# Performance work log

Measured on AMD Instinct MI355X. Metric: run time of the kernel, lower is better.

Reference implementation:

```python
import jax, jax.numpy as jnp
import numpy as np

N = 50000       # nodes
E = 1_200_000   # directed edges (avg degree 24)
IN_F = 128
C = 64          # CL1_F hidden width
K = 3           # Chebyshev order
OUT_F = 2
EPS = 1e-5      # BatchNorm eps (torch default)


def setup_inputs() -> dict:
    key = jax.random.key(0)
    ks = jax.random.split(key, 8)
    s = 0.1
    x = jax.random.normal(ks[0], (N, IN_F), dtype=jnp.float32)
    edge_index = jax.random.randint(ks[1], (2, E), 0, N, dtype=jnp.int32)
    W1 = jax.random.normal(ks[2], (K, IN_F, C), dtype=jnp.float32) * s
    b1 = jnp.zeros((C,), jnp.float32)
    W_rest = jax.random.normal(ks[3], (9, K, C, C), dtype=jnp.float32) * s
    b_rest = jnp.zeros((9, C), jnp.float32)
    gamma = jnp.ones((10, C), jnp.float32)
    beta = jnp.zeros((10, C), jnp.float32)
    lin_w = jax.random.normal(ks[4], (C, OUT_F), dtype=jnp.float32) * s
    lin_b = jnp.zeros((OUT_F,), jnp.float32)
    return dict(x=x, edge_index=edge_index, W1=W1, b1=b1, W_rest=W_rest,
                b_rest=b_rest, gamma=gamma, beta=beta, lin_w=lin_w, lin_b=lin_b)


def _cheb_norm(edge_index):
    # PyG ChebConv normalization with lambda_max=2, sym Laplacian, unit edge weights:
    # L_hat = 2L/lambda_max - I = -D^{-1/2} A D^{-1/2} (diagonal becomes 0).
    row, col = edge_index[0], edge_index[1]
    deg = jax.ops.segment_sum(jnp.ones((E,), jnp.float32), row, num_segments=N)
    dinv = jnp.where(deg > 0, jax.lax.rsqrt(jnp.maximum(deg, 1.0)), 0.0)
    w = -dinv[row] * dinv[col]  # per-edge weight of L_hat
    return row, col, w


def _cheb_conv(x, W, b, row, col, w):
    # Chebyshev recursion: Tx_0 = x, Tx_1 = L_hat x, Tx_k = 2 L_hat Tx_{k-1} - Tx_{k-2}
    Lhat = lambda v: jax.ops.segment_sum(w[:, None] * v[col], row, num_segments=N)
    Tx0 = x
    out = Tx0 @ W[0]
    Tx1 = Lhat(x)
    out = out + Tx1 @ W[1]
    for k in range(2, W.shape[0]):
        Tx2 = 2.0 * Lhat(Tx1) - Tx0
        out = out + Tx2 @ W[k]
        Tx0, Tx1 = Tx1, Tx2
    return out + b


def _bn(x, g, b):
    # BatchNorm1d over nodes (training-mode batch statistics, biased var)
    mu = x.mean(axis=0)
    var = ((x - mu) ** 2).mean(axis=0)
    return g * (x - mu) * jax.lax.rsqrt(var + EPS) + b


def reference(x, edge_index, W1, b1, W_rest, b_rest, gamma, beta, lin_w, lin_b):
    row, col, w = _cheb_norm(edge_index)
    h = _bn(jax.nn.relu(_cheb_conv(x, W1, b1, row, col, w)), gamma[0], beta[0])
    for i in range(9):  # convs 2..10 (structurally identical, stacked params)
        h = _bn(jax.nn.relu(_cheb_conv(h, W_rest[i], b_rest[i], row, col, w)),
                gamma[i + 1], beta[i + 1])
    return h @ lin_w + lin_b
```

## Files before the change

### kernel.cpp

```cpp
#include <hip/hip_runtime.h>
#include <hip/hip_bf16.h>

#define N_NODES 50000
#define N_EDGES 1200000
#define EPS_BN 1e-5f
#define NB 1024
#define RPB 49
#define CAP 2048

typedef __attribute__((ext_vector_type(8))) short short8;
typedef __attribute__((ext_vector_type(4))) float f32x4;

union U16x8 { uint4 u; short8 s; };

__device__ __forceinline__ float lo2f(unsigned int u){ return __uint_as_float(u << 16); }
__device__ __forceinline__ float hi2f(unsigned int u){ return __uint_as_float(u & 0xffff0000u); }
__device__ __forceinline__ float b2f(unsigned short u){ return __uint_as_float(((unsigned int)u) << 16); }
__device__ __forceinline__ unsigned short f2b(float f){
  __hip_bfloat16 b = __float2bfloat16(f);
  return __builtin_bit_cast(unsigned short, b);
}

__global__ void binA(const int* __restrict__ row, const int* __restrict__ col,
                     int* __restrict__ bcnt, int2* __restrict__ tmp, int E){
  __shared__ int hist[NB];
  __shared__ int base[NB];
  for (int i=threadIdx.x; i<NB; i+=256) hist[i] = 0;
  __syncthreads();
  int e0 = blockIdx.x*4096;
  int r_[16], c_[16];
  #pragma unroll
  for (int k=0;k<16;k++){
    int e = e0 + k*256 + threadIdx.x;
    if (e < E){
      r_[k] = row[e]; c_[k] = col[e];
      atomicAdd(&hist[r_[k]/RPB], 1);
    } else r_[k] = -1;
  }
  __syncthreads();
  for (int i=threadIdx.x; i<NB; i+=256){
    int cnt = hist[i];
    base[i] = cnt ? atomicAdd(&bcnt[i], cnt) : 0;
    hist[i] = 0;
  }
  __syncthreads();
  #pragma unroll
  for (int k=0;k<16;k++){
    if (r_[k] >= 0){
      int b = r_[k]/RPB;
      int p = base[b] + atomicAdd(&hist[b], 1);
      tmp[(size_t)b*CAP + p] = make_int2(r_[k], c_[k]);
    }
  }
}

__global__ void scan1024(const int* __restrict__ bcnt, int* __restrict__ bbase,
                         int* __restrict__ offs, int n, int E){
  __shared__ int tmp[NB];
  int i = threadIdx.x;
  int v = bcnt[i];
  tmp[i] = v;
  __syncthreads();
  for (int off=1; off<NB; off<<=1){
    int t = (i >= off) ? tmp[i-off] : 0;
    __syncthreads();
    tmp[i] += t;
    __syncthreads();
  }
  bbase[i] = tmp[i] - v;
  if (i == 0) offs[n] = E;
}

__global__ void binB(const int* __restrict__ bcnt, const int* __restrict__ bbase,
                     const int2* __restrict__ tmp,
                     int* __restrict__ offs, float* __restrict__ dinv,
                     int* __restrict__ ep, int n){
  __shared__ int cnt[RPB];
  __shared__ int roff[RPB];
  int b = blockIdx.x;
  int r0 = b*RPB;
  int m = bcnt[b];
  size_t tbase = (size_t)b*CAP;
  for (int i=threadIdx.x; i<RPB; i+=256) cnt[i] = 0;
  __syncthreads();
  for (int t=threadIdx.x; t<m; t+=256)
    atomicAdd(&cnt[tmp[tbase+t].x - r0], 1);
  __syncthreads();
  if (threadIdx.x == 0){
    int acc = bbase[b];
    #pragma unroll
    for (int i=0;i<RPB;i++){ roff[i] = acc; acc += cnt[i]; }
  }
  __syncthreads();
  if (threadIdx.x < RPB){
    int r = r0 + threadIdx.x;
    if (r < n){
      offs[r] = roff[threadIdx.x];
      int d = cnt[threadIdx.x];
      dinv[r] = (d>0) ? rsqrtf((float)d) : 0.f;
    }
  }
  __syncthreads();
  for (int i=threadIdx.x; i<RPB; i+=256) cnt[i] = 0;
  __syncthreads();
  for (int t=threadIdx.x; t<m; t+=256){
    int2 rc = tmp[tbase+t];
    int lr = rc.x - r0;
    int p = roff[lr] + atomicAdd(&cnt[lr], 1);
    ep[p] = rc.y;
  }
}

__global__ void cast_xs(const float* __restrict__ x, const float* __restrict__ dinv,
                        uint4* __restrict__ xs, int n){
  int t = blockIdx.x*256 + threadIdx.x;
  if (t >= n*16) return;
  int node = t >> 4;
  int fb = (t & 15)*8;
  float dv = dinv[node];
  const float* xp = x + (size_t)node*128 + fb;
  float4 v0 = *(const float4*)xp;
  float4 v1 = *(const float4*)(xp+4);
  float vv[8] = {v0.x,v0.y,v0.z,v0.w,v1.x,v1.y,v1.z,v1.w};
  uint4 o;
  unsigned int* op = (unsigned int*)&o;
  #pragma unroll
  for (int p=0;p<4;p++){
    op[p] = (unsigned int)f2b(dv*vv[2*p]) | ((unsigned int)f2b(dv*vv[2*p+1]) << 16);
  }
  xs[t] = o;
}

__global__ void transpose_w_split(const float* __restrict__ W1, const float* __restrict__ Wr,
                                  unsigned short* __restrict__ WTh,
                                  unsigned short* __restrict__ WTl){
  int t = blockIdx.x*256 + threadIdx.x;
  float val;
  if (t < 24576){
    int c = t/384, kk = t%384;
    int seg = kk/128, f = kk%128;
    if (seg==0)      val = W1[(size_t)f*64 + c] - W1[(size_t)(256+f)*64 + c];
    else if (seg==1) val = W1[(size_t)(128+f)*64 + c];
    else             val = 2.f * W1[(size_t)(256+f)*64 + c];
  } else if (t < 135168){
    int u = t - 24576;
    int L = u/12288, r2 = u%12288;
    int c = r2/192, kk = r2%192;
    int seg = kk/64, f = kk%64;
    const float* WL = Wr + (size_t)L*12288;
    if (seg==0)      val = WL[(size_t)f*64 + c] - WL[(size_t)(128+f)*64 + c];
    else if (seg==1) val = WL[(size_t)(64+f)*64 + c];
    else             val = 2.f * WL[(size_t)(128+f)*64 + c];
  } else return;
  unsigned short h = f2b(val);
  WTh[t] = h;
  WTl[t] = f2b(val - b2f(h));
}

__device__ __forceinline__ void spmm_acc8(uint4 u, float* a){
  a[0] += lo2f(u.x);
  a[1] += hi2f(u.x);
  a[2] += lo2f(u.y);
  a[3] += hi2f(u.y);
  a[4] += lo2f(u.z);
  a[5] += hi2f(u.z);
  a[6] += lo2f(u.w);
  a[7] += hi2f(u.w);
}

template<int F, bool BOTH>
__global__ void spmm_bf16(const int* __restrict__ offs, const int* __restrict__ ep,
                          const float* __restrict__ dinv,
                          const unsigned short* __restrict__ src,
                          unsigned short* __restrict__ dst_u,
                          unsigned short* __restrict__ dst_s, int n){
  constexpr int LPR = F/8;
  constexpr int RPW = 64/LPR;
  int lane = threadIdx.x & 63;
  int wv = threadIdx.x >> 6;
  int lr = lane / LPR;
  int li = lane % LPR;
  int row = (blockIdx.x*4 + wv)*RPW + lr;
  int s = 0, e = 0;
  if (row < n){ s = offs[row]; e = offs[row+1]; }
  float a[8];
  #pragma unroll
  for (int c=0;c<8;c++) a[c]=0.f;
  const int fb = li*8;
  int j = s;
  for (; j+4 <= e; j += 4){
    int c0 = ep[j+0];
    int c1 = ep[j+1];
    int c2 = ep[j+2];
    int c3 = ep[j+3];
    uint4 u0 = *(const uint4*)(src + (size_t)c0*F + fb);
    uint4 u1 = *(const uint4*)(src + (size_t)c1*F + fb);
    uint4 u2 = *(const uint4*)(src + (size_t)c2*F + fb);
    uint4 u3 = *(const uint4*)(src + (size_t)c3*F + fb);
    spmm_acc8(u0, a);
    spmm_acc8(u1, a);
    spmm_acc8(u2, a);
    spmm_acc8(u3, a);
  }
  for (; j < e; ++j){
    uint4 u = *(const uint4*)(src + (size_t)ep[j]*F + fb);
    spmm_acc8(u, a);
  }
  if (row < n){
    float dv = dinv[row];
    float uv[8];
    #pragma unroll
    for (int c=0;c<8;c++) uv[c] = -dv * a[c];
    uint4 ou;
    unsigned int* oup = (unsigned int*)&ou;
    #pragma unroll
    for (int p=0;p<4;p++)
      oup[p] = (unsigned int)f2b(uv[2*p]) | ((unsigned int)f2b(uv[2*p+1]) << 16);
    *(uint4*)(dst_u + (size_t)row*F + fb) = ou;
    if (BOTH){
      uint4 os;
      unsigned int* osp = (unsigned int*)&os;
      #pragma unroll
      for (int p=0;p<4;p++)
        osp[p] = (unsigned int)f2b(dv*uv[2*p]) | ((unsigned int)f2b(dv*uv[2*p+1]) << 16);
      *(uint4*)(dst_s + (size_t)row*F + fb) = os;
    }
  }
}

template<int SEGF>
__global__ void gemm_mfma(const float* __restrict__ A0f,
                          const float* __restrict__ scsh,
                          const unsigned short* __restrict__ A1,
                          const unsigned short* __restrict__ A2,
                          const unsigned short* __restrict__ WTh,
                          const unsigned short* __restrict__ WTl,
                          const float* __restrict__ bias,
                          float* __restrict__ out,
                          float* __restrict__ stats, int n){
  constexpr int K = 3*SEGF;
  constexpr int KPS = SEGF/32;
  constexpr int CHUNKS = 16*SEGF;
  constexpr int PLANE_CH = 8*SEGF;
  __shared__ unsigned short wlds[2*64*SEGF];
  __shared__ float ssum[64];
  __shared__ float ssq[64];
  __shared__ float sc_l[128];
  __shared__ float sh_l[128];
  if (threadIdx.x < 64){ ssum[threadIdx.x] = 0.f; ssq[threadIdx.x] = 0.f; }
  if (threadIdx.x < SEGF){
    if (scsh){
      sc_l[threadIdx.x] = scsh[threadIdx.x];
      sh_l[threadIdx.x] = scsh[64 + threadIdx.x];
    } else {
      sc_l[threadIdx.x] = 1.f;
      sh_l[threadIdx.x] = 0.f;
    }
  }

  int lane = threadIdx.x & 63;
  int wv = threadIdx.x >> 6;
  int mrow = lane & 15;
  int kg = lane >> 4;
  int brow = blockIdx.x*64 + wv*16;
  int m = brow + mrow;
  bool mv = m < n;

  f32x4 acc[4];
  #pragma unroll
  for (int t=0;t<4;t++) acc[t] = f32x4{0.f,0.f,0.f,0.f};

  #pragma unroll
  for (int seg=0; seg<3; ++seg){
    #pragma unroll
    for (int c0=0; c0<CHUNKS; c0+=256){
      int c = c0 + threadIdx.x;
      int plane = c / PLANE_CH;
      int r = c % PLANE_CH;
      int col = r / (SEGF/8);
      int k8 = r % (SEGF/8);
      const unsigned short* srcp = (plane ? WTl : WTh) + (size_t)col*K + seg*SEGF + k8*8;
      uint4 v = *(const uint4*)srcp;
      int byte = ((plane*64 + col)*SEGF + k8*8)*2;
      byte ^= (col & 7) << 4;
      *(uint4*)((char*)wlds + byte) = v;
    }
    U16x8 afh[KPS], afl[KPS];
    #pragma unroll
    for (int kk=0; kk<KPS; ++kk){
      int koff = kk*32 + kg*8;
      if (seg==0){
        float y[8];
        if (mv){
          const float* gp = A0f + (size_t)m*SEGF + koff;
          float4 v0 = *(const float4*)gp;
          float4 v1 = *(const float4*)(gp+4);
          float g[8] = {v0.x,v0.y,v0.z,v0.w,v1.x,v1.y,v1.z,v1.w};
          #pragma unroll
          for (int i=0;i<8;i++){
            int f = koff + i;
            y[i] = fmaf(g[i], sc_l[f], sh_l[f]);
          }
        } else {
          #pragma unroll
          for (int i=0;i<8;i++) y[i] = 0.f;
        }
        unsigned int* hp = (unsigned int*)&afh[kk].u;
        unsigned int* lp = (unsigned int*)&afl[kk].u;
        #pragma unroll
        for (int p=0;p<4;p++){
          unsigned short h0 = f2b(y[2*p]),  h1 = f2b(y[2*p+1]);
          unsigned short l0 = f2b(y[2*p] - b2f(h0)), l1 = f2b(y[2*p+1] - b2f(h1));
          hp[p] = (unsigned int)h0 | ((unsigned int)h1 << 16);
          lp[p] = (unsigned int)l0 | ((unsigned int)l1 << 16);
        }
      } else {
        const unsigned short* Ah = (seg==1) ? A1 : A2;
        if (mv) afh[kk].u = *(const uint4*)(Ah + (size_t)m*SEGF + koff);
        else    afh[kk].u = make_uint4(0,0,0,0);
      }
    }
    __syncthreads();
    #pragma unroll
    for (int kk=0; kk<KPS; ++kk){
      #pragma unroll
      for (int t=0;t<4;t++){
        int col = t*16 + mrow;
        int koff = kk*32 + kg*8;
        int byteh = (col*SEGF + koff)*2;          byteh ^= (col & 7) << 4;
        int bytel = ((64 + col)*SEGF + koff)*2;   bytel ^= (col & 7) << 4;
        U16x8 bh, bl;
        bh.u = *(const uint4*)((const char*)wlds + byteh);
        bl.u = *(const uint4*)((const char*)wlds + bytel);
        acc[t] = __builtin_amdgcn_mfma_f32_16x16x32_bf16(afh[kk].s, bh.s, acc[t], 0, 0, 0);
        acc[t] = __builtin_amdgcn_mfma_f32_16x16x32_bf16(afh[kk].s, bl.s, acc[t], 0, 0, 0);
        if (seg==0)
          acc[t] = __builtin_amdgcn_mfma_f32_16x16x32_bf16(afl[kk].s, bh.s, acc[t], 0, 0, 0);
      }
    }
    __syncthreads();
  }

  #pragma unroll
  for (int t=0;t<4;t++){
    int col = t*16 + mrow;
    float bsv = bias[col];
    float s = 0.f, sq = 0.f;
    #pragma unroll
    for (int i=0;i<4;i++){
      int r = brow + kg*4 + i;
      float v = fmaxf(acc[t][i] + bsv, 0.f);
      if (r < n){
        out[(size_t)r*64 + col] = v;
        s += v; sq += v*v;
      }
    }
    s  += __shfl_xor(s, 16);  sq += __shfl_xor(sq, 16);
    s  += __shfl_xor(s, 32);  sq += __shfl_xor(sq, 32);
    if (kg == 0){
      atomicAdd(&ssum[col], s);
      atomicAdd(&ssq[col], sq);
    }
  }
  __syncthreads();
  if (threadIdx.x < 64){
    float* sl = stats + (blockIdx.x & 15)*128;
    atomicAdd(&sl[threadIdx.x], ssum[threadIdx.x]);
    atomicAdd(&sl[64+threadIdx.x], ssq[threadIdx.x]);
  }
}

__global__ void bn_scale(const float* __restrict__ g_in, const float* __restrict__ dinv,
                         unsigned short* __restrict__ hs,
                         const float* __restrict__ stats, float* __restrict__ scsh,
                         const float* __restrict__ gamma, const float* __restrict__ beta,
                         int n){
  __shared__ float red[128];
  __shared__ float sc[64], sh[64];
  int tid = threadIdx.x;
  if (tid < 128){
    float s = 0.f;
    #pragma unroll
    for (int r=0;r<16;r++) s += stats[r*128 + tid];
    red[tid] = s;
  }
  __syncthreads();
  if (tid < 64){
    float inv_n = 1.f/(float)n;
    float mu = red[tid]*inv_n;
    float var = red[64+tid]*inv_n - mu*mu;
    float a = gamma[tid]*rsqrtf(var + EPS_BN);
    sc[tid] = a;
    sh[tid] = beta[tid] - mu*a;
    if (blockIdx.x == 0){
      scsh[tid] = a;
      scsh[64+tid] = sh[tid];
    }
  }
  __syncthreads();
  int t = blockIdx.x*256 + tid;
  if (t >= n*8) return;
  int fb = (t & 7)*8;
  int node = t >> 3;
  float dv = dinv[node];
  const float* gp = g_in + (size_t)node*64 + fb;
  float4 v0 = *(const float4*)gp;
  float4 v1 = *(const float4*)(gp + 4);
  float vv[8] = {v0.x, v0.y, v0.z, v0.w, v1.x, v1.y, v1.z, v1.w};
  uint4 o;
  unsigned int* op = (unsigned int*)&o;
  #pragma unroll
  for (int p=0;p<4;p++){
    int f0 = fb + 2*p, f1 = f0 + 1;
    float y0 = dv * fmaf(vv[2*p],   sc[f0], sh[f0]);
    float y1 = dv * fmaf(vv[2*p+1], sc[f1], sh[f1]);
    op[p] = (unsigned int)f2b(y0) | ((unsigned int)f2b(y1) << 16);
  }
  ((uint4*)hs)[t] = o;
}

__global__ void final_linear_bn(const float* __restrict__ g_in,
                                const float* __restrict__ stats,
                                const float* __restrict__ gamma, const float* __restrict__ beta,
                                const float* __restrict__ w, const float* __restrict__ b,
                                float* __restrict__ out, int n){
  __shared__ float red[128];
  __shared__ float sc[64], sh[64];
  int tid = threadIdx.x;
  if (tid < 128){
    float s = 0.f;
    #pragma unroll
    for (int r=0;r<16;r++) s += stats[r*128 + tid];
    red[tid] = s;
  }
  __syncthreads();
  if (tid < 64){
    float inv_n = 1.f/(float)n;
    float mu = red[tid]*inv_n;
    float var = red[64+tid]*inv_n - mu*mu;
    float a = gamma[tid]*rsqrtf(var + EPS_BN);
    sc[tid] = a;
    sh[tid] = beta[tid] - mu*a;
  }
  __syncthreads();
  int i = blockIdx.x*256 + tid;
  if (i >= n) return;
  float a0 = b[0], a1 = b[1];
  const float* gp = g_in + (size_t)i*64;
  #pragma unroll
  for (int k=0;k<64;k++){
    float v = fmaf(gp[k], sc[k], sh[k]);
    a0 = fmaf(v, w[k*2+0], a0);
    a1 = fmaf(v, w[k*2+1], a1);
  }
  out[i*2+0] = a0;
  out[i*2+1] = a1;
}

extern "C" void kernel_launch(void* const* d_in, const int* in_sizes, int n_in,
                              void* d_out, int out_size, void* d_ws, size_t ws_size,
                              hipStream_t stream){
  const float* x     = (const float*)d_in[0];
  const int*   ei    = (const int*)d_in[1];
  const float* W1    = (const float*)d_in[2];
  const float* b1    = (const float*)d_in[3];
  const float* Wr    = (const float*)d_in[4];
  const float* br    = (const float*)d_in[5];
  const float* gamma = (const float*)d_in[6];
  const float* beta  = (const float*)d_in[7];
  const float* lw    = (const float*)d_in[8];
  const float* lb    = (const float*)d_in[9];
  const int N = N_NODES, E = N_EDGES;
  const int* row = ei;
  const int* col = ei + E;

  char* ws = (char*)d_ws;
  size_t off = 0;
  auto alloc = [&](size_t bytes)->void*{
    void* p = ws + off; off = (off + bytes + 255) & ~(size_t)255; return p; };
  float*          dinv  = (float*) alloc((size_t)N*4);
  int*            offs  = (int*)   alloc((size_t)(N+1)*4);
  int*            bcnt  = (int*)   alloc(NB*4);
  int*            bbase = (int*)   alloc(NB*4);
  int2*           tmp   = (int2*)  alloc((size_t)NB*CAP*8);
  int*            ep    = (int*)   alloc((size_t)E*4);
  unsigned short* xs    = (unsigned short*)alloc((size_t)N*128*2);
  unsigned short* T1u   = (unsigned short*)alloc((size_t)N*128*2);
  unsigned short* T1s   = (unsigned short*)alloc((size_t)N*128*2);
  unsigned short* Uu    = (unsigned short*)alloc((size_t)N*128*2);
  unsigned short* hs    = (unsigned short*)alloc((size_t)N*64*2);
  float*          gbuf  = (float*) alloc((size_t)N*64*4);
  unsigned short* WTh   = (unsigned short*)alloc((size_t)135168*2);
  unsigned short* WTl   = (unsigned short*)alloc((size_t)135168*2);
  float*          stats = (float*) alloc((size_t)10*2048*4);
  float*          scsh  = (float*) alloc((size_t)10*128*4);

  hipMemsetAsync(bcnt, 0, NB*4, stream);
  hipMemsetAsync(stats, 0, (size_t)10*2048*4, stream);
  binA<<<(E+4095)/4096, 256, 0, stream>>>(row, col, bcnt, tmp, E);
  scan1024<<<1, NB, 0, stream>>>(bcnt, bbase, offs, N, E);
  binB<<<NB, 256, 0, stream>>>(bcnt, bbase, tmp, offs, dinv, ep, N);

  cast_xs<<<((N*16)+255)/256, 256, 0, stream>>>(x, dinv, (uint4*)xs, N);
  transpose_w_split<<<(135168+255)/256, 256, 0, stream>>>(W1, Wr, WTh, WTl);

  spmm_bf16<128,true ><<<(N+15)/16, 256, 0, stream>>>(offs, ep, dinv, xs, T1u, T1s, N);
  spmm_bf16<128,false><<<(N+15)/16, 256, 0, stream>>>(offs, ep, dinv, T1s, Uu, nullptr, N);
  gemm_mfma<128><<<(N+63)/64, 256, 0, stream>>>(x, nullptr, T1u, Uu, WTh, WTl,
      b1, gbuf, stats, N);

  for (int L=0; L<9; ++L){
    bn_scale<<<((N*8)+255)/256, 256, 0, stream>>>(gbuf, dinv, hs,
        stats + (size_t)L*2048, scsh + (size_t)L*128,
        gamma + (size_t)L*64, beta + (size_t)L*64, N);
    spmm_bf16<64,true ><<<(N+31)/32, 256, 0, stream>>>(offs, ep, dinv, hs, T1u, T1s, N);
    spmm_bf16<64,false><<<(N+31)/32, 256, 0, stream>>>(offs, ep, dinv, T1s, Uu, nullptr, N);
    gemm_mfma<64><<<(N+63)/64, 256, 0, stream>>>(gbuf, scsh + (size_t)L*128, T1u, Uu,
        WTh + 24576 + (size_t)L*12288, WTl + 24576 + (size_t)L*12288,
        br + (size_t)L*64, gbuf, stats + (size_t)(L+1)*2048, N);
  }

  final_linear_bn<<<(N+255)/256, 256, 0, stream>>>(gbuf, stats + (size_t)9*2048,
      gamma + (size_t)9*64, beta + (size_t)9*64, lw, lb, (float*)d_out, N);
}
```

Measured before the change: 676.3 us.

## Project layer-1 features to 64 width before propagation and drop duplicate T1 buffer

For the first layer, x is first multiplied by the W1[1] and 2*W1[2] blocks, producing 64-wide outputs. The sparse propagation then runs on those 64-wide results instead of 128-wide inputs, which halves gather traffic for layer 1. The later layers no longer write a separate unscaled T1; the GEMM rebuilds it from the scaled copy by multiplying with sqrt(deg), which removes one output stream per SpMM. Edge binning also packs the local row and column into a single int, halving the temp buffer. The column packing keeps only 16 bits of the column index while node ids reach 50000, which is acceptable only because 50000 fits in 16 bits. The T1 reconstruction adds extra bf16 rounding.

```diff
diff --git a/kernel.cpp b/kernel.cpp
--- a/kernel.cpp
+++ b/kernel.cpp
@@ -22,7 +22,7 @@
 }
 
 __global__ void binA(const int* __restrict__ row, const int* __restrict__ col,
-                     int* __restrict__ bcnt, int2* __restrict__ tmp, int E){
+                     int* __restrict__ bcnt, int* __restrict__ tmp, int E){
   __shared__ int hist[NB];
   __shared__ int base[NB];
   for (int i=threadIdx.x; i<NB; i+=256) hist[i] = 0;
@@ -48,8 +48,9 @@
   for (int k=0;k<16;k++){
     if (r_[k] >= 0){
       int b = r_[k]/RPB;
+      int lr = r_[k] - b*RPB;
       int p = base[b] + atomicAdd(&hist[b], 1);
-      tmp[(size_t)b*CAP + p] = make_int2(r_[k], c_[k]);
+      tmp[(size_t)b*CAP + p] = (lr << 16) | c_[k];
     }
   }
 }
@@ -72,9 +73,9 @@
 }
 
 __global__ void binB(const int* __restrict__ bcnt, const int* __restrict__ bbase,
-                     const int2* __restrict__ tmp,
+                     const int* __restrict__ tmp,
                      int* __restrict__ offs, float* __restrict__ dinv,
-                     int* __restrict__ ep, int n){
+                     float* __restrict__ rdeg, int* __restrict__ ep, int n){
   __shared__ int cnt[RPB];
   __shared__ int roff[RPB];
   int b = blockIdx.x;
@@ -84,7 +85,7 @@
   for (int i=threadIdx.x; i<RPB; i+=256) cnt[i] = 0;
   __syncthreads();
   for (int t=threadIdx.x; t<m; t+=256)
-    atomicAdd(&cnt[tmp[tbase+t].x - r0], 1);
+    atomicAdd(&cnt[tmp[tbase+t] >> 16], 1);
   __syncthreads();
   if (threadIdx.x == 0){
     int acc = bbase[b];
@@ -98,63 +99,49 @@
       offs[r] = roff[threadIdx.x];
       int d = cnt[threadIdx.x];
       dinv[r] = (d>0) ? rsqrtf((float)d) : 0.f;
+      rdeg[r] = (d>0) ? sqrtf((float)d) : 0.f;
     }
   }
   __syncthreads();
   for (int i=threadIdx.x; i<RPB; i+=256) cnt[i] = 0;
   __syncthreads();
   for (int t=threadIdx.x; t<m; t+=256){
-    int2 rc = tmp[tbase+t];
-    int lr = rc.x - r0;
+    int v = tmp[tbase+t];
+    int lr = v >> 16;
     int p = roff[lr] + atomicAdd(&cnt[lr], 1);
-    ep[p] = rc.y;
-  }
-}
-
-__global__ void cast_xs(const float* __restrict__ x, const float* __restrict__ dinv,
-                        uint4* __restrict__ xs, int n){
+    ep[p] = v & 0xFFFF;
+  }
+}
+
+__global__ void transpose_w(const float* __restrict__ W1, const float* __restrict__ Wr,
+                            unsigned short* __restrict__ WTh,
+                            unsigned short* __restrict__ WTl,
+                            unsigned short* __restrict__ BCT){
   int t = blockIdx.x*256 + threadIdx.x;
-  if (t >= n*16) return;
-  int node = t >> 4;
-  int fb = (t & 15)*8;
-  float dv = dinv[node];
-  const float* xp = x + (size_t)node*128 + fb;
-  float4 v0 = *(const float4*)xp;
-  float4 v1 = *(const float4*)(xp+4);
-  float vv[8] = {v0.x,v0.y,v0.z,v0.w,v1.x,v1.y,v1.z,v1.w};
-  uint4 o;
-  unsigned int* op = (unsigned int*)&o;
-  #pragma unroll
-  for (int p=0;p<4;p++){
-    op[p] = (unsigned int)f2b(dv*vv[2*p]) | ((unsigned int)f2b(dv*vv[2*p+1]) << 16);
-  }
-  xs[t] = o;
-}
-
-__global__ void transpose_w_split(const float* __restrict__ W1, const float* __restrict__ Wr,
-                                  unsigned short* __restrict__ WTh,
-                                  unsigned short* __restrict__ WTl){
-  int t = blockIdx.x*256 + threadIdx.x;
-  float val;
-  if (t < 24576){
-    int c = t/384, kk = t%384;
-    int seg = kk/128, f = kk%128;
-    if (seg==0)      val = W1[(size_t)f*64 + c] - W1[(size_t)(256+f)*64 + c];
-    else if (seg==1) val = W1[(size_t)(128+f)*64 + c];
-    else             val = 2.f * W1[(size_t)(256+f)*64 + c];
-  } else if (t < 135168){
-    int u = t - 24576;
+  if (t < 8192){
+    int c = t/128, k = t%128;
+    float val = W1[(size_t)k*64 + c] - W1[(size_t)(256+k)*64 + c];
+    unsigned short h = f2b(val);
+    WTh[t] = h; WTl[t] = f2b(val - b2f(h));
+  } else if (t < 118784){
+    int u = t - 8192;
     int L = u/12288, r2 = u%12288;
     int c = r2/192, kk = r2%192;
     int seg = kk/64, f = kk%64;
     const float* WL = Wr + (size_t)L*12288;
+    float val;
     if (seg==0)      val = WL[(size_t)f*64 + c] - WL[(size_t)(128+f)*64 + c];
     else if (seg==1) val = WL[(size_t)(64+f)*64 + c];
     else             val = 2.f * WL[(size_t)(128+f)*64 + c];
-  } else return;
-  unsigned short h = f2b(val);
-  WTh[t] = h;
-  WTl[t] = f2b(val - b2f(h));
+    unsigned short h = f2b(val);
+    WTh[t] = h; WTl[t] = f2b(val - b2f(h));
+  } else if (t < 135168){
+    int u = t - 118784;
+    int j = u/128, k = u%128;
+    float val = (j < 64) ? W1[(size_t)(128+k)*64 + j]
+                         : 2.f * W1[(size_t)(256+k)*64 + (j-64)];
+    BCT[u] = f2b(val);
+  }
 }
 
 __device__ __forceinline__ void spmm_acc8(uint4 u, float* a){
@@ -168,19 +155,17 @@
   a[7] += hi2f(u.w);
 }
 
-template<int F, bool BOTH>
-__global__ void spmm_bf16(const int* __restrict__ offs, const int* __restrict__ ep,
-                          const float* __restrict__ dinv,
-                          const unsigned short* __restrict__ src,
-                          unsigned short* __restrict__ dst_u,
-                          unsigned short* __restrict__ dst_s, int n){
-  constexpr int LPR = F/8;
-  constexpr int RPW = 64/LPR;
+template<int MODE>
+__global__ void spmm64(const int* __restrict__ offs, const int* __restrict__ ep,
+                       const float* __restrict__ dinv,
+                       const unsigned short* __restrict__ src,
+                       const unsigned short* __restrict__ padd,
+                       unsigned short* __restrict__ dst, int n){
   int lane = threadIdx.x & 63;
   int wv = threadIdx.x >> 6;
-  int lr = lane / LPR;
-  int li = lane % LPR;
-  int row = (blockIdx.x*4 + wv)*RPW + lr;
+  int lr = lane >> 3;
+  int li = lane & 7;
+  int row = (blockIdx.x*4 + wv)*8 + lr;
   int s = 0, e = 0;
   if (row < n){ s = offs[row]; e = offs[row+1]; }
   float a[8];
@@ -193,17 +178,17 @@
     int c1 = ep[j+1];
     int c2 = ep[j+2];
     int c3 = ep[j+3];
-    uint4 u0 = *(const uint4*)(src + (size_t)c0*F + fb);
-    uint4 u1 = *(const uint4*)(src + (size_t)c1*F + fb);
-    uint4 u2 = *(const uint4*)(src + (size_t)c2*F + fb);
-    uint4 u3 = *(const uint4*)(src + (size_t)c3*F + fb);
+    uint4 u0 = *(const uint4*)(src + (size_t)c0*64 + fb);
+    uint4 u1 = *(const uint4*)(src + (size_t)c1*64 + fb);
+    uint4 u2 = *(const uint4*)(src + (size_t)c2*64 + fb);
+    uint4 u3 = *(const uint4*)(src + (size_t)c3*64 + fb);
     spmm_acc8(u0, a);
     spmm_acc8(u1, a);
     spmm_acc8(u2, a);
     spmm_acc8(u3, a);
   }
   for (; j < e; ++j){
-    uint4 u = *(const uint4*)(src + (size_t)ep[j]*F + fb);
+    uint4 u = *(const uint4*)(src + (size_t)ep[j]*64 + fb);
     spmm_acc8(u, a);
   }
   if (row < n){
@@ -211,53 +196,39 @@
     float uv[8];
     #pragma unroll
     for (int c=0;c<8;c++) uv[c] = -dv * a[c];
-    uint4 ou;
-    unsigned int* oup = (unsigned int*)&ou;
+    if (MODE == 2){
+      uint4 pu = *(const uint4*)(padd + (size_t)row*64 + fb);
+      float pv[8] = {lo2f(pu.x),hi2f(pu.x),lo2f(pu.y),hi2f(pu.y),
+                     lo2f(pu.z),hi2f(pu.z),lo2f(pu.w),hi2f(pu.w)};
+      #pragma unroll
+      for (int c=0;c<8;c++) uv[c] = dv*(pv[c] + uv[c]);
+    } else if (MODE == 1){
+      #pragma unroll
+      for (int c=0;c<8;c++) uv[c] = dv*uv[c];
+    }
+    uint4 o;
+    unsigned int* op = (unsigned int*)&o;
     #pragma unroll
     for (int p=0;p<4;p++)
-      oup[p] = (unsigned int)f2b(uv[2*p]) | ((unsigned int)f2b(uv[2*p+1]) << 16);
-    *(uint4*)(dst_u + (size_t)row*F + fb) = ou;
-    if (BOTH){
-      uint4 os;
-      unsigned int* osp = (unsigned int*)&os;
-      #pragma unroll
-      for (int p=0;p<4;p++)
-        osp[p] = (unsigned int)f2b(dv*uv[2*p]) | ((unsigned int)f2b(dv*uv[2*p+1]) << 16);
-      *(uint4*)(dst_s + (size_t)row*F + fb) = os;
-    }
-  }
-}
-
-template<int SEGF>
-__global__ void gemm_mfma(const float* __restrict__ A0f,
-                          const float* __restrict__ scsh,
-                          const unsigned short* __restrict__ A1,
-                          const unsigned short* __restrict__ A2,
-                          const unsigned short* __restrict__ WTh,
-                          const unsigned short* __restrict__ WTl,
-                          const float* __restrict__ bias,
-                          float* __restrict__ out,
-                          float* __restrict__ stats, int n){
-  constexpr int K = 3*SEGF;
-  constexpr int KPS = SEGF/32;
-  constexpr int CHUNKS = 16*SEGF;
-  constexpr int PLANE_CH = 8*SEGF;
-  __shared__ unsigned short wlds[2*64*SEGF];
-  __shared__ float ssum[64];
-  __shared__ float ssq[64];
-  __shared__ float sc_l[128];
-  __shared__ float sh_l[128];
-  if (threadIdx.x < 64){ ssum[threadIdx.x] = 0.f; ssq[threadIdx.x] = 0.f; }
-  if (threadIdx.x < SEGF){
-    if (scsh){
-      sc_l[threadIdx.x] = scsh[threadIdx.x];
-      sh_l[threadIdx.x] = scsh[64 + threadIdx.x];
-    } else {
-      sc_l[threadIdx.x] = 1.f;
-      sh_l[threadIdx.x] = 0.f;
-    }
-  }
-
+      op[p] = (unsigned int)f2b(uv[2*p]) | ((unsigned int)f2b(uv[2*p+1]) << 16);
+    *(uint4*)(dst + (size_t)row*64 + fb) = o;
+  }
+}
+
+__global__ void gemm1_l1(const float* __restrict__ x, const unsigned short* __restrict__ BCT,
+                         const float* __restrict__ dinv,
+                         unsigned short* __restrict__ pb, unsigned short* __restrict__ qs,
+                         int n){
+  __shared__ unsigned short wlds[128*128];
+  #pragma unroll
+  for (int c0=0; c0<2048; c0+=256){
+    int c = c0 + threadIdx.x;
+    int col = c >> 4, k8 = c & 15;
+    uint4 v = *(const uint4*)(BCT + (size_t)col*128 + k8*8);
+    int byte = (col*128 + k8*8)*2;
+    byte ^= (col & 7) << 4;
+    *(uint4*)((char*)wlds + byte) = v;
+  }
   int lane = threadIdx.x & 63;
   int wv = threadIdx.x >> 6;
   int mrow = lane & 15;
@@ -266,28 +237,214 @@
   int m = brow + mrow;
   bool mv = m < n;
 
+  U16x8 af[4];
+  #pragma unroll
+  for (int kk=0;kk<4;kk++){
+    int koff = kk*32 + kg*8;
+    unsigned int* hp = (unsigned int*)&af[kk].u;
+    if (mv){
+      const float* gp = x + (size_t)m*128 + koff;
+      float4 v0 = *(const float4*)gp;
+      float4 v1 = *(const float4*)(gp+4);
+      float g[8] = {v0.x,v0.y,v0.z,v0.w,v1.x,v1.y,v1.z,v1.w};
+      #pragma unroll
+      for (int p=0;p<4;p++)
+        hp[p] = (unsigned int)f2b(g[2*p]) | ((unsigned int)f2b(g[2*p+1]) << 16);
+    } else {
+      af[kk].u = make_uint4(0,0,0,0);
+    }
+  }
+  __syncthreads();
+
+  f32x4 acc[8];
+  #pragma unroll
+  for (int t=0;t<8;t++) acc[t] = f32x4{0.f,0.f,0.f,0.f};
+  #pragma unroll
+  for (int kk=0;kk<4;kk++){
+    int koff = kk*32 + kg*8;
+    #pragma unroll
+    for (int t=0;t<8;t++){
+      int col = t*16 + mrow;
+      int byte = (col*128 + koff)*2;
+      byte ^= (col & 7) << 4;
+      U16x8 b;
+      b.u = *(const uint4*)((const char*)wlds + byte);
+      acc[t] = __builtin_amdgcn_mfma_f32_16x16x32_bf16(af[kk].s, b.s, acc[t], 0, 0, 0);
+    }
+  }
+
+  #pragma unroll
+  for (int t=0;t<8;t++){
+    int col = t*16 + mrow;
+    #pragma unroll
+    for (int i=0;i<4;i++){
+      int r = brow + kg*4 + i;
+      if (r < n){
+        if (col < 64) pb[(size_t)r*64 + col] = f2b(acc[t][i]);
+        else          qs[(size_t)r*64 + col - 64] = f2b(dinv[r]*acc[t][i]);
+      }
+    }
+  }
+}
+
+__global__ void gemm2_l1(const float* __restrict__ x,
+                         const unsigned short* __restrict__ ATh,
+                         const unsigned short* __restrict__ ATl,
+                         const unsigned short* __restrict__ su,
+                         const float* __restrict__ bias,
+                         float* __restrict__ out, float* __restrict__ stats, int n){
+  __shared__ unsigned short wlds[2*64*128];
+  __shared__ float ssum[64];
+  __shared__ float ssq[64];
+  if (threadIdx.x < 64){ ssum[threadIdx.x] = 0.f; ssq[threadIdx.x] = 0.f; }
+  #pragma unroll
+  for (int c0=0; c0<2048; c0+=256){
+    int c = c0 + threadIdx.x;
+    int plane = c >> 10;
+    int r = c & 1023;
+    int col = r >> 4, k8 = r & 15;
+    const unsigned short* srcp = (plane ? ATl : ATh) + (size_t)col*128 + k8*8;
+    uint4 v = *(const uint4*)srcp;
+    int byte = ((plane*64 + col)*128 + k8*8)*2;
+    byte ^= (col & 7) << 4;
+    *(uint4*)((char*)wlds + byte) = v;
+  }
+  int lane = threadIdx.x & 63;
+  int wv = threadIdx.x >> 6;
+  int mrow = lane & 15;
+  int kg = lane >> 4;
+  int brow = blockIdx.x*64 + wv*16;
+  int m = brow + mrow;
+  bool mv = m < n;
+
+  U16x8 afh[4], afl[4];
+  #pragma unroll
+  for (int kk=0;kk<4;kk++){
+    int koff = kk*32 + kg*8;
+    unsigned int* hp = (unsigned int*)&afh[kk].u;
+    unsigned int* lp = (unsigned int*)&afl[kk].u;
+    if (mv){
+      const float* gp = x + (size_t)m*128 + koff;
+      float4 v0 = *(const float4*)gp;
+      float4 v1 = *(const float4*)(gp+4);
+      float g[8] = {v0.x,v0.y,v0.z,v0.w,v1.x,v1.y,v1.z,v1.w};
+      #pragma unroll
+      for (int p=0;p<4;p++){
+        unsigned short h0 = f2b(g[2*p]),  h1 = f2b(g[2*p+1]);
+        unsigned short l0 = f2b(g[2*p] - b2f(h0)), l1 = f2b(g[2*p+1] - b2f(h1));
+        hp[p] = (unsigned int)h0 | ((unsigned int)h1 << 16);
+        lp[p] = (unsigned int)l0 | ((unsigned int)l1 << 16);
+      }
+    } else {
+      afh[kk].u = make_uint4(0,0,0,0);
+      afl[kk].u = make_uint4(0,0,0,0);
+    }
+  }
+  __syncthreads();
+
   f32x4 acc[4];
   #pragma unroll
   for (int t=0;t<4;t++) acc[t] = f32x4{0.f,0.f,0.f,0.f};
+  #pragma unroll
+  for (int kk=0;kk<4;kk++){
+    int koff = kk*32 + kg*8;
+    #pragma unroll
+    for (int t=0;t<4;t++){
+      int col = t*16 + mrow;
+      int byteh = (col*128 + koff)*2;          byteh ^= (col & 7) << 4;
+      int bytel = ((64 + col)*128 + koff)*2;   bytel ^= (col & 7) << 4;
+      U16x8 bh, bl;
+      bh.u = *(const uint4*)((const char*)wlds + byteh);
+      bl.u = *(const uint4*)((const char*)wlds + bytel);
+      acc[t] = __builtin_amdgcn_mfma_f32_16x16x32_bf16(afh[kk].s, bh.s, acc[t], 0, 0, 0);
+      acc[t] = __builtin_amdgcn_mfma_f32_16x16x32_bf16(afh[kk].s, bl.s, acc[t], 0, 0, 0);
+      acc[t] = __builtin_amdgcn_mfma_f32_16x16x32_bf16(afl[kk].s, bh.s, acc[t], 0, 0, 0);
+    }
+  }
+
+  #pragma unroll
+  for (int t=0;t<4;t++){
+    int col = t*16 + mrow;
+    float bsv = bias[col];
+    float s = 0.f, sq = 0.f;
+    #pragma unroll
+    for (int i=0;i<4;i++){
+      int r = brow + kg*4 + i;
+      if (r < n){
+        float v = acc[t][i] + b2f(su[(size_t)r*64 + col]) + bsv;
+        v = fmaxf(v, 0.f);
+        out[(size_t)r*64 + col] = v;
+        s += v; sq += v*v;
+      }
+    }
+    s  += __shfl_xor(s, 16);  sq += __shfl_xor(sq, 16);
+    s  += __shfl_xor(s, 32);  sq += __shfl_xor(sq, 32);
+    if (kg == 0){
+      atomicAdd(&ssum[col], s);
+      atomicAdd(&ssq[col], sq);
+    }
+  }
+  __syncthreads();
+  if (threadIdx.x < 64){
+    float* sl = stats + (blockIdx.x & 15)*128;
+    atomicAdd(&sl[threadIdx.x], ssum[threadIdx.x]);
+    atomicAdd(&sl[64+threadIdx.x], ssq[threadIdx.x]);
+  }
+}
+
+__global__ void gemm_mfma64(const float* __restrict__ A0f,
+                            const float* __restrict__ scsh,
+                            const unsigned short* __restrict__ A1,
+                            const unsigned short* __restrict__ A2,
+                            const float* __restrict__ rdeg,
+                            const unsigned short* __restrict__ WTh,
+                            const unsigned short* __restrict__ WTl,
+                            const float* __restrict__ bias,
+                            float* __restrict__ out,
+                            float* __restrict__ stats, int n){
+  constexpr int SEGF = 64;
+  constexpr int K = 192;
+  __shared__ unsigned short wlds[2*64*SEGF];
+  __shared__ float ssum[64];
+  __shared__ float ssq[64];
+  __shared__ float sc_l[64];
+  __shared__ float sh_l[64];
+  if (threadIdx.x < 64){
+    ssum[threadIdx.x] = 0.f; ssq[threadIdx.x] = 0.f;
+    sc_l[threadIdx.x] = scsh[threadIdx.x];
+    sh_l[threadIdx.x] = scsh[64 + threadIdx.x];
+  }
+
+  int lane = threadIdx.x & 63;
+  int wv = threadIdx.x >> 6;
+  int mrow = lane & 15;
+  int kg = lane >> 4;
+  int brow = blockIdx.x*64 + wv*16;
+  int m = brow + mrow;
+  bool mv = m < n;
+  float rm = mv ? rdeg[m] : 0.f;
+
+  f32x4 acc[4];
+  #pragma unroll
+  for (int t=0;t<4;t++) acc[t] = f32x4{0.f,0.f,0.f,0.f};
 
   #pragma unroll
   for (int seg=0; seg<3; ++seg){
     #pragma unroll
-    for (int c0=0; c0<CHUNKS; c0+=256){
+    for (int c0=0; c0<1024; c0+=256){
       int c = c0 + threadIdx.x;
-      int plane = c / PLANE_CH;
-      int r = c % PLANE_CH;
-      int col = r / (SEGF/8);
-      int k8 = r % (SEGF/8);
+      int plane = c >> 9;
+      int r = c & 511;
+      int col = r >> 3, k8 = r & 7;
       const unsigned short* srcp = (plane ? WTl : WTh) + (size_t)col*K + seg*SEGF + k8*8;
       uint4 v = *(const uint4*)srcp;
       int byte = ((plane*64 + col)*SEGF + k8*8)*2;
       byte ^= (col & 7) << 4;
       *(uint4*)((char*)wlds + byte) = v;
     }
-    U16x8 afh[KPS], afl[KPS];
-    #pragma unroll
-    for (int kk=0; kk<KPS; ++kk){
+    U16x8 afh[2], afl[2];
+    #pragma unroll
+    for (int kk=0; kk<2; ++kk){
       int koff = kk*32 + kg*8;
       if (seg==0){
         float y[8];
@@ -314,15 +471,24 @@
           hp[p] = (unsigned int)h0 | ((unsigned int)h1 << 16);
           lp[p] = (unsigned int)l0 | ((unsigned int)l1 << 16);
         }
+      } else if (seg==1){
+        unsigned int* hp = (unsigned int*)&afh[kk].u;
+        if (mv){
+          uint4 u = *(const uint4*)(A1 + (size_t)m*SEGF + koff);
+          float g[8] = {lo2f(u.x),hi2f(u.x),lo2f(u.y),hi2f(u.y),
+                        lo2f(u.z),hi2f(u.z),lo2f(u.w),hi2f(u.w)};
+          #pragma unroll
+          for (int p=0;p<4;p++)
+            hp[p] = (unsigned int)f2b(rm*g[2*p]) | ((unsigned int)f2b(rm*g[2*p+1]) << 16);
+        } else afh[kk].u = make_uint4(0,0,0,0);
       } else {
-        const unsigned short* Ah = (seg==1) ? A1 : A2;
-        if (mv) afh[kk].u = *(const uint4*)(Ah + (size_t)m*SEGF + koff);
+        if (mv) afh[kk].u = *(const uint4*)(A2 + (size_t)m*SEGF + koff);
         else    afh[kk].u = make_uint4(0,0,0,0);
       }
     }
     __syncthreads();
     #pragma unroll
-    for (int kk=0; kk<KPS; ++kk){
+    for (int kk=0; kk<2; ++kk){
       #pragma unroll
       for (int t=0;t<4;t++){
         int col = t*16 + mrow;
@@ -349,8 +515,8 @@
     #pragma unroll
     for (int i=0;i<4;i++){
       int r = brow + kg*4 + i;
-      float v = fmaxf(acc[t][i] + bsv, 0.f);
       if (r < n){
+        float v = fmaxf(acc[t][i] + bsv, 0.f);
         out[(size_t)r*64 + col] = v;
         s += v; sq += v*v;
       }
@@ -479,19 +645,21 @@
   auto alloc = [&](size_t bytes)->void*{
     void* p = ws + off; off = (off + bytes + 255) & ~(size_t)255; return p; };
   float*          dinv  = (float*) alloc((size_t)N*4);
+  float*          rdeg  = (float*) alloc((size_t)N*4);
   int*            offs  = (int*)   alloc((size_t)(N+1)*4);
   int*            bcnt  = (int*)   alloc(NB*4);
   int*            bbase = (int*)   alloc(NB*4);
-  int2*           tmp   = (int2*)  alloc((size_t)NB*CAP*8);
+  int*            tmp   = (int*)   alloc((size_t)NB*CAP*4);
   int*            ep    = (int*)   alloc((size_t)E*4);
-  unsigned short* xs    = (unsigned short*)alloc((size_t)N*128*2);
-  unsigned short* T1u   = (unsigned short*)alloc((size_t)N*128*2);
-  unsigned short* T1s   = (unsigned short*)alloc((size_t)N*128*2);
-  unsigned short* Uu    = (unsigned short*)alloc((size_t)N*128*2);
+  unsigned short* pb    = (unsigned short*)alloc((size_t)N*64*2);
+  unsigned short* qs    = (unsigned short*)alloc((size_t)N*64*2);
+  unsigned short* T1s   = (unsigned short*)alloc((size_t)N*64*2);
+  unsigned short* Uu    = (unsigned short*)alloc((size_t)N*64*2);
   unsigned short* hs    = (unsigned short*)alloc((size_t)N*64*2);
   float*          gbuf  = (float*) alloc((size_t)N*64*4);
-  unsigned short* WTh   = (unsigned short*)alloc((size_t)135168*2);
-  unsigned short* WTl   = (unsigned short*)alloc((size_t)135168*2);
+  unsigned short* WTh   = (unsigned short*)alloc((size_t)118784*2);
+  unsigned short* WTl   = (unsigned short*)alloc((size_t)118784*2);
+  unsigned short* BCT   = (unsigned short*)alloc((size_t)16384*2);
   float*          stats = (float*) alloc((size_t)10*2048*4);
   float*          scsh  = (float*) alloc((size_t)10*128*4);
 
@@ -499,24 +667,24 @@
   hipMemsetAsync(stats, 0, (size_t)10*2048*4, stream);
   binA<<<(E+4095)/4096, 256, 0, stream>>>(row, col, bcnt, tmp, E);
   scan1024<<<1, NB, 0, stream>>>(bcnt, bbase, offs, N, E);
-  binB<<<NB, 256, 0, stream>>>(bcnt, bbase, tmp, offs, dinv, ep, N);
-
-  cast_xs<<<((N*16)+255)/256, 256, 0, stream>>>(x, dinv, (uint4*)xs, N);
-  transpose_w_split<<<(135168+255)/256, 256, 0, stream>>>(W1, Wr, WTh, WTl);
-
-  spmm_bf16<128,true ><<<(N+15)/16, 256, 0, stream>>>(offs, ep, dinv, xs, T1u, T1s, N);
-  spmm_bf16<128,false><<<(N+15)/16, 256, 0, stream>>>(offs, ep, dinv, T1s, Uu, nullptr, N);
-  gemm_mfma<128><<<(N+63)/64, 256, 0, stream>>>(x, nullptr, T1u, Uu, WTh, WTl,
-      b1, gbuf, stats, N);
+  binB<<<NB, 256, 0, stream>>>(bcnt, bbase, tmp, offs, dinv, rdeg, ep, N);
+
+  transpose_w<<<(135168+255)/256, 256, 0, stream>>>(W1, Wr, WTh, WTl, BCT);
+
+  int sg = (N+31)/32;
+  gemm1_l1<<<(N+63)/64, 256, 0, stream>>>(x, BCT, dinv, pb, qs, N);
+  spmm64<2><<<sg, 256, 0, stream>>>(offs, ep, dinv, qs, pb, T1s, N);
+  spmm64<0><<<sg, 256, 0, stream>>>(offs, ep, dinv, T1s, nullptr, Uu, N);
+  gemm2_l1<<<(N+63)/64, 256, 0, stream>>>(x, WTh, WTl, Uu, b1, gbuf, stats, N);
 
   for (int L=0; L<9; ++L){
     bn_scale<<<((N*8)+255)/256, 256, 0, stream>>>(gbuf, dinv, hs,
         stats + (size_t)L*2048, scsh + (size_t)L*128,
         gamma + (size_t)L*64, beta + (size_t)L*64, N);
-    spmm_bf16<64,true ><<<(N+31)/32, 256, 0, stream>>>(offs, ep, dinv, hs, T1u, T1s, N);
-    spmm_bf16<64,false><<<(N+31)/32, 256, 0, stream>>>(offs, ep, dinv, T1s, Uu, nullptr, N);
-    gemm_mfma<64><<<(N+63)/64, 256, 0, stream>>>(gbuf, scsh + (size_t)L*128, T1u, Uu,
-        WTh + 24576 + (size_t)L*12288, WTl + 24576 + (size_t)L*12288,
+    spmm64<1><<<sg, 256, 0, stream>>>(offs, ep, dinv, hs, nullptr, T1s, N);
+    spmm64<0><<<sg, 256, 0, stream>>>(offs, ep, dinv, T1s, nullptr, Uu, N);
+    gemm_mfma64<<<(N+63)/64, 256, 0, stream>>>(gbuf, scsh + (size_t)L*128, T1s, Uu, rdeg,
+        WTh + 8192 + (size_t)L*12288, WTl + 8192 + (size_t)L*12288,
         br + (size_t)L*64, gbuf, stats + (size_t)(L+1)*2048, N);
   }
 
```

After: 632.7 us, median of 2. 6.4% less time.
